# Kernel optimization log

Hardware: AMD Instinct MI355X
Metric: run time of the kernel (lower is better)

Reference implementation:

```python
import jax, jax.numpy as jnp
import numpy as np


def _rconv(x, w, b):
    # reflection-pad 1 then 3x3 valid conv (same spatial size), NCHW/OIHW
    xp = jnp.pad(x, ((0, 0), (0, 0), (1, 1), (1, 1)), mode='reflect')
    y = jax.lax.conv_general_dilated(
        xp, w, window_strides=(1, 1), padding='VALID',
        dimension_numbers=('NCHW', 'OIHW', 'NCHW'))
    return y + b[None, :, None, None]


def setup_inputs() -> dict:
    key = jax.random.key(0)
    ks = jax.random.split(key, 12)
    B, C, H, W = 4, 256, 64, 64
    IC = 128  # inter_channels
    s = lambda fan_in: 1.0 / np.sqrt(fan_in)
    return {
        'query_feat': jax.random.normal(ks[0], (B, C, H, W), jnp.float32),
        'key_feat': jax.random.normal(ks[1], (B, C, H, W), jnp.float32),
        # 1x1 conv projections (stored as [out, in])
        'w_theta': jax.random.normal(ks[2], (IC, C), jnp.float32) * s(C),
        'b_theta': jnp.zeros((IC,), jnp.float32),
        'w_phi': jax.random.normal(ks[3], (IC, C), jnp.float32) * s(C),
        'b_phi': jnp.zeros((IC,), jnp.float32),
        # post-correlation block: conv(1->32), residual(32), conv(32->1)
        'w_in': jax.random.normal(ks[4], (32, 1, 3, 3), jnp.float32) * s(9),
        'b_in': jnp.zeros((32,), jnp.float32),
        'w_r1': jax.random.normal(ks[5], (32, 32, 3, 3), jnp.float32) * s(32 * 9),
        'b_r1': jnp.zeros((32,), jnp.float32),
        'w_r2': jax.random.normal(ks[6], (32, 32, 3, 3), jnp.float32) * s(32 * 9),
        'b_r2': jnp.zeros((32,), jnp.float32),
        'w_out': jax.random.normal(ks[7], (1, 32, 3, 3), jnp.float32) * s(32 * 9),
        'b_out': jnp.zeros((1,), jnp.float32),
    }


def reference(query_feat, key_feat, w_theta, b_theta, w_phi, b_phi,
              w_in, b_in, w_r1, b_r1, w_r2, b_r2, w_out, b_out):
    B, C, H, W = query_feat.shape
    N = H * W
    # 1x1 conv projections, flattened to sequences
    theta = jnp.einsum('oc,bchw->bohw', w_theta, query_feat) + b_theta[None, :, None, None]
    phi = jnp.einsum('oc,bchw->bohw', w_phi, key_feat) + b_phi[None, :, None, None]
    theta = theta.reshape(B, -1, N).transpose(0, 2, 1)  # [B, N, IC]
    phi = phi.reshape(B, -1, N)                          # [B, IC, N]
    # correlation matrix [B, N, N] then max over key positions
    f = jnp.matmul(theta, phi)
    sim = jnp.max(f, axis=-1).reshape(B, 1, H, W)
    # post-correlation conv refinement
    h = _rconv(sim, w_in, b_in)                      # 1 -> 32
    r = jax.nn.relu(_rconv(h, w_r1, b_r1))           # residual block
    r = _rconv(r, w_r2, b_r2)
    h = h + r
    out = _rconv(h, w_out, b_out)                    # 32 -> 1
    return out
```

## Files before the change

### kernel.cpp

```cpp
#include <hip/hip_runtime.h>

#define B_ 4
#define C_ 256
#define HH 64
#define WW 64
#define N_ 4096
#define IC_ 128
#define JC_ 8

typedef __attribute__((ext_vector_type(8))) short bf16x8;
typedef __attribute__((ext_vector_type(4))) float f32x4;

__device__ __forceinline__ short f2bf(float f) {
    unsigned u = __builtin_bit_cast(unsigned, f);
    unsigned r = (u + 0x7FFFu + ((u >> 16) & 1u)) >> 16;
    return (short)r;
}

__device__ __forceinline__ int refl(int v) {
    return v < 0 ? -v : (v > 63 ? 126 - v : v);
}

__global__ __launch_bounds__(256) void k_cvt_w(const float* __restrict__ wt,
                                               const float* __restrict__ wp,
                                               short* __restrict__ wtb,
                                               short* __restrict__ wpb) {
    int i = blockIdx.x * 256 + threadIdx.x;
    wtb[i] = f2bf(wt[i]);
    wpb[i] = f2bf(wp[i]);
}

__global__ __launch_bounds__(256) void k_project(
    const float* __restrict__ qf, const float* __restrict__ kf,
    const short* __restrict__ wq, const short* __restrict__ wk,
    const float* __restrict__ bq, const float* __restrict__ bk,
    short* __restrict__ outq, short* __restrict__ outk) {
    int z = blockIdx.z;
    const float* x = z ? kf : qf;
    const short* wbf = z ? wk : wq;
    const float* bias = z ? bk : bq;
    short* outT = z ? outk : outq;

    int b = blockIdx.y;
    int n0 = blockIdx.x * 64;
    int t = threadIdx.x;
    int lane = t & 63, wv = t >> 6;
    int l15 = lane & 15, q4 = lane >> 4;
    const float* xb = x + (size_t)b * C_ * N_;

    __shared__ float xs[2][32][65];

    f32x4 acc[8];
#pragma unroll
    for (int cf = 0; cf < 8; cf++) acc[cf] = (f32x4){0.f, 0.f, 0.f, 0.f};

    {
        int i0 = t, i1 = t + 256;
        int r0 = i0 >> 4, c0 = i0 & 15;
        int r1 = i1 >> 4, c1 = i1 & 15;
        f32x4 v0 = *(const f32x4*)(xb + (size_t)r0 * N_ + n0 + c0 * 4);
        f32x4 v1 = *(const f32x4*)(xb + (size_t)r1 * N_ + n0 + c1 * 4);
#pragma unroll
        for (int s = 0; s < 4; s++) xs[0][r0][c0 * 4 + s] = v0[s];
#pragma unroll
        for (int s = 0; s < 4; s++) xs[0][r1][c1 * 4 + s] = v1[s];
    }

    for (int ks = 0; ks < 8; ks++) {
        __syncthreads();
        int buf = ks & 1;
        if (ks < 7) {
            int cb = (ks + 1) * 32;
            int i0 = t, i1 = t + 256;
            int r0 = i0 >> 4, c0 = i0 & 15;
            int r1 = i1 >> 4, c1 = i1 & 15;
            f32x4 v0 = *(const f32x4*)(xb + (size_t)(cb + r0) * N_ + n0 + c0 * 4);
            f32x4 v1 = *(const f32x4*)(xb + (size_t)(cb + r1) * N_ + n0 + c1 * 4);
#pragma unroll
            for (int s = 0; s < 4; s++) xs[buf ^ 1][r0][c0 * 4 + s] = v0[s];
#pragma unroll
            for (int s = 0; s < 4; s++) xs[buf ^ 1][r1][c1 * 4 + s] = v1[s];
        }
        int cbase = ks * 32 + q4 * 8;
        bf16x8 a;
#pragma unroll
        for (int j = 0; j < 8; j++) a[j] = f2bf(xs[buf][q4 * 8 + j][wv * 16 + l15]);
#pragma unroll
        for (int cf = 0; cf < 8; cf++) {
            const short* wp = wbf + (cf * 16 + l15) * C_ + cbase;
            bf16x8 bfr = *(const bf16x8*)wp;
            acc[cf] = __builtin_amdgcn_mfma_f32_16x16x32_bf16(a, bfr, acc[cf], 0, 0, 0);
        }
    }
#pragma unroll
    for (int cf = 0; cf < 8; cf++) {
        int ic = cf * 16 + l15;
        float bv = bias[ic];
#pragma unroll
        for (int r = 0; r < 4; r++) {
            int n = n0 + wv * 16 + q4 * 4 + r;
            outT[((size_t)b * N_ + n) * IC_ + ic] = f2bf(acc[cf][r] + bv);
        }
    }
}

__global__ __launch_bounds__(256, 4) void k_corr(const short* __restrict__ thetaT,
                                                 const short* __restrict__ phiT,
                                                 float* __restrict__ simp) {
    __shared__ short ph[2][64][136];

    int b = blockIdx.z, jc = blockIdx.y;
    int i0 = blockIdx.x * 128;
    int t = threadIdx.x;
    int lane = t & 63, w = t >> 6;
    int l15 = lane & 15, q4 = lane >> 4;

    const short* thb = thetaT + ((size_t)b * N_ + i0 + w * 32) * IC_;
    const short* phb = phiT + ((size_t)b * N_ + jc * (N_ / JC_)) * IC_;

    bf16x8 afr[2][4];
#pragma unroll
    for (int rf = 0; rf < 2; rf++)
#pragma unroll
        for (int ks = 0; ks < 4; ks++)
            afr[rf][ks] = *(const bf16x8*)(thb + (size_t)(rf * 16 + l15) * IC_ + ks * 32 + q4 * 8);

    int srow = t >> 4, sc8 = t & 15;
#pragma unroll
    for (int k = 0; k < 4; k++)
        *(bf16x8*)(&ph[0][srow + k * 16][sc8 * 8]) =
            *(const bf16x8*)(phb + (size_t)(srow + k * 16) * IC_ + sc8 * 8);

    f32x4 rmax[2];
#pragma unroll
    for (int rf = 0; rf < 2; rf++) rmax[rf] = (f32x4){-3.0e38f, -3.0e38f, -3.0e38f, -3.0e38f};

    const int NT = (N_ / JC_) / 64;
    for (int it = 0; it < NT; it++) {
        int buf = it & 1;
        __syncthreads();
        if (it < NT - 1) {
            int j0 = (it + 1) * 64;
#pragma unroll
            for (int k = 0; k < 4; k++)
                *(bf16x8*)(&ph[buf ^ 1][srow + k * 16][sc8 * 8]) =
                    *(const bf16x8*)(phb + (size_t)(j0 + srow + k * 16) * IC_ + sc8 * 8);
        }
#pragma unroll
        for (int jf = 0; jf < 4; jf++) {
            bf16x8 bfr[4];
#pragma unroll
            for (int ks = 0; ks < 4; ks++)
                bfr[ks] = *(const bf16x8*)(&ph[buf][jf * 16 + l15][ks * 32 + q4 * 8]);
#pragma unroll
            for (int rf = 0; rf < 2; rf++) {
                f32x4 a2 = (f32x4){0.f, 0.f, 0.f, 0.f};
#pragma unroll
                for (int ks = 0; ks < 4; ks++)
                    a2 = __builtin_amdgcn_mfma_f32_16x16x32_bf16(afr[rf][ks], bfr[ks], a2, 0, 0, 0);
#pragma unroll
                for (int r = 0; r < 4; r++) rmax[rf][r] = fmaxf(rmax[rf][r], a2[r]);
            }
        }
    }

#pragma unroll
    for (int rf = 0; rf < 2; rf++) {
#pragma unroll
        for (int r = 0; r < 4; r++) {
            float v = rmax[rf][r];
            v = fmaxf(v, __shfl_xor(v, 1));
            v = fmaxf(v, __shfl_xor(v, 2));
            v = fmaxf(v, __shfl_xor(v, 4));
            v = fmaxf(v, __shfl_xor(v, 8));
            rmax[rf][r] = v;
        }
    }
    if (l15 == 0) {
        float* sp = simp + ((size_t)(b * JC_ + jc)) * N_ + i0 + w * 32;
#pragma unroll
        for (int rf = 0; rf < 2; rf++)
#pragma unroll
            for (int r = 0; r < 4; r++) sp[rf * 16 + q4 * 4 + r] = rmax[rf][r];
    }
}

__global__ __launch_bounds__(256) void k_conv_in(const float* __restrict__ simp,
                                                 const float* __restrict__ w,
                                                 const float* __restrict__ bias,
                                                 float* __restrict__ h) {
    int y = blockIdx.x, b = blockIdx.y;
    int t = threadIdx.x;
    int oc = t >> 3, x8 = t & 7;
    __shared__ float srow[3][66];
    const float* sb = simp + (size_t)b * JC_ * N_;
    if (t < 192) {
        int r = t >> 6, x = t & 63;
        int idx = refl(y - 1 + r) * 64 + x;
        float v = -3.0e38f;
#pragma unroll
        for (int jc = 0; jc < JC_; jc++) v = fmaxf(v, sb[jc * N_ + idx]);
        srow[r][x + 1] = v;
    }
    if (t < 3) {
        int gy = refl(y - 1 + t);
        float vl = -3.0e38f, vr = -3.0e38f;
#pragma unroll
        for (int jc = 0; jc < JC_; jc++) {
            vl = fmaxf(vl, sb[jc * N_ + gy * 64 + 1]);
            vr = fmaxf(vr, sb[jc * N_ + gy * 64 + 62]);
        }
        srow[t][0] = vl;
        srow[t][65] = vr;
    }
    __syncthreads();

    float wr[9];
#pragma unroll
    for (int k = 0; k < 9; k++) wr[k] = w[oc * 9 + k];
    float bv = bias[oc];
    float acc[8];
#pragma unroll
    for (int xi = 0; xi < 8; xi++) acc[xi] = bv;
#pragma unroll
    for (int ky = 0; ky < 3; ky++)
#pragma unroll
        for (int kx = 0; kx < 3; kx++) {
            float wv2 = wr[ky * 3 + kx];
#pragma unroll
            for (int xi = 0; xi < 8; xi++) acc[xi] += wv2 * srow[ky][x8 * 8 + xi + kx];
        }
    float* op = h + (((size_t)b * 32 + oc) * 64 + y) * 64 + x8 * 8;
#pragma unroll
    for (int xi = 0; xi < 8; xi++) op[xi] = acc[xi];
}

template <bool RELU, bool ADD>
__global__ __launch_bounds__(256) void k_conv_r(const float* __restrict__ in,
                                                const float* __restrict__ w,
                                                const float* __restrict__ bias,
                                                float* __restrict__ out,
                                                const float* __restrict__ add) {
    int y = blockIdx.x, b = blockIdx.z;
    int oc0 = blockIdx.y * 16;
    int t = threadIdx.x;
    __shared__ float tile[32][3][68];

#pragma unroll
    for (int r = 0; r < 3; r++) {
        int gy = refl(y - 1 + r);
#pragma unroll
        for (int i = 0; i < 2; i++) {
            int idx = t + i * 256;
            int ic = idx >> 4, c4 = idx & 15;
            f32x4 v = *(const f32x4*)(in + (((size_t)b * 32 + ic) * 64 + gy) * 64 + c4 * 4);
#pragma unroll
            for (int s = 0; s < 4; s++) tile[ic][r][c4 * 4 + s + 1] = v[s];
        }
    }
    if (t < 96) {
        int ic = t / 3, r = t - ic * 3;
        int gy = refl(y - 1 + r);
        const float* row = in + (((size_t)b * 32 + ic) * 64 + gy) * 64;
        tile[ic][r][0] = row[1];
        tile[ic][r][65] = row[62];
    }
    __syncthreads();

    int oc = oc0 + (t >> 4), x4 = (t & 15) * 4;
    float bv = bias[oc];
    float acc[4];
#pragma unroll
    for (int xi = 0; xi < 4; xi++) acc[xi] = bv;

    for (int ic = 0; ic < 32; ic++) {
        const float* wp = w + ((size_t)oc * 32 + ic) * 9;
        float w0 = wp[0], w1 = wp[1], w2 = wp[2], w3 = wp[3], w4 = wp[4];
        float w5 = wp[5], w6 = wp[6], w7 = wp[7], w8 = wp[8];
        float xr[3][8];
#pragma unroll
        for (int r = 0; r < 3; r++) {
            const float* rowp = &tile[ic][r][x4];
            f32x4 A = *(const f32x4*)(rowp);
            f32x4 Bv = *(const f32x4*)(rowp + 4);
            xr[r][0] = A[0]; xr[r][1] = A[1]; xr[r][2] = A[2]; xr[r][3] = A[3];
            xr[r][4] = Bv[0]; xr[r][5] = Bv[1]; xr[r][6] = Bv[2]; xr[r][7] = Bv[3];
        }
#pragma unroll
        for (int xi = 0; xi < 4; xi++) {
            acc[xi] += w0 * xr[0][xi] + w1 * xr[0][xi + 1] + w2 * xr[0][xi + 2] +
                       w3 * xr[1][xi] + w4 * xr[1][xi + 1] + w5 * xr[1][xi + 2] +
                       w6 * xr[2][xi] + w7 * xr[2][xi + 1] + w8 * xr[2][xi + 2];
        }
    }
    size_t off = (((size_t)b * 32 + oc) * 64 + y) * 64 + x4;
#pragma unroll
    for (int xi = 0; xi < 4; xi++) {
        float v = acc[xi];
        if (RELU) v = fmaxf(v, 0.f);
        if (ADD) v += add[off + xi];
        out[off + xi] = v;
    }
}

__global__ __launch_bounds__(256) void k_conv_out(const float* __restrict__ hb,
                                                  const float* __restrict__ w,
                                                  const float* __restrict__ bias,
                                                  float* __restrict__ outp) {
    int y = blockIdx.x, b = blockIdx.y;
    int t = threadIdx.x;
    int x = t & 63, g = t >> 6;
    __shared__ float red[4][64];
    float acc = 0.f;
#pragma unroll
    for (int i = 0; i < 8; i++) {
        int ic = g * 8 + i;
        const float* wp = w + ic * 9;
#pragma unroll
        for (int ky = 0; ky < 3; ky++) {
            int gy = refl(y + ky - 1);
            const float* row = hb + (((size_t)b * 32 + ic) * 64 + gy) * 64;
#pragma unroll
            for (int kx = 0; kx < 3; kx++) {
                int gx = refl(x + kx - 1);
                acc += wp[ky * 3 + kx] * row[gx];
            }
        }
    }
    red[g][x] = acc;
    __syncthreads();
    if (t < 64) {
        outp[((size_t)b * 64 + y) * 64 + x] =
            bias[0] + red[0][t] + red[1][t] + red[2][t] + red[3][t];
    }
}

extern "C" void kernel_launch(void* const* d_in, const int* in_sizes, int n_in,
                              void* d_out, int out_size, void* d_ws, size_t ws_size,
                              hipStream_t stream) {
    const float* q = (const float*)d_in[0];
    const float* kf = (const float*)d_in[1];
    const float* w_theta = (const float*)d_in[2];
    const float* b_theta = (const float*)d_in[3];
    const float* w_phi = (const float*)d_in[4];
    const float* b_phi = (const float*)d_in[5];
    const float* w_in = (const float*)d_in[6];
    const float* b_in = (const float*)d_in[7];
    const float* w_r1 = (const float*)d_in[8];
    const float* b_r1 = (const float*)d_in[9];
    const float* w_r2 = (const float*)d_in[10];
    const float* b_r2 = (const float*)d_in[11];
    const float* w_out = (const float*)d_in[12];
    const float* b_out = (const float*)d_in[13];
    float* out = (float*)d_out;

    char* ws = (char*)d_ws;
    short* thetaT = (short*)(ws);
    short* phiT = (short*)(ws + 4194304);
    short* wthb = (short*)(ws + 8388608);
    short* wphb = (short*)(ws + 8454144);
    float* simp = (float*)(ws + 8519680);
    float* h = (float*)(ws);
    float* r = (float*)(ws + 2097152);

    k_cvt_w<<<128, 256, 0, stream>>>(w_theta, w_phi, wthb, wphb);
    k_project<<<dim3(64, 4, 2), 256, 0, stream>>>(q, kf, wthb, wphb, b_theta, b_phi,
                                                  thetaT, phiT);
    k_corr<<<dim3(32, JC_, 4), 256, 0, stream>>>(thetaT, phiT, simp);
    k_conv_in<<<dim3(64, 4), 256, 0, stream>>>(simp, w_in, b_in, h);
    k_conv_r<true, false><<<dim3(64, 2, 4), 256, 0, stream>>>(h, w_r1, b_r1, r, nullptr);
    k_conv_r<false, true><<<dim3(64, 2, 4), 256, 0, stream>>>(r, w_r2, b_r2, h, h);
    k_conv_out<<<dim3(64, 4), 256, 0, stream>>>(h, w_out, b_out, out);
}
```

Measured before the change: 167.5 us.

## Fuse weight bf16 conversion into projection and stage conv weights in LDS

```diff
diff --git a/kernel.cpp b/kernel.cpp
--- a/kernel.cpp
+++ b/kernel.cpp
@@ -21,23 +21,14 @@
     return v < 0 ? -v : (v > 63 ? 126 - v : v);
 }
 
-__global__ __launch_bounds__(256) void k_cvt_w(const float* __restrict__ wt,
-                                               const float* __restrict__ wp,
-                                               short* __restrict__ wtb,
-                                               short* __restrict__ wpb) {
-    int i = blockIdx.x * 256 + threadIdx.x;
-    wtb[i] = f2bf(wt[i]);
-    wpb[i] = f2bf(wp[i]);
-}
-
 __global__ __launch_bounds__(256) void k_project(
     const float* __restrict__ qf, const float* __restrict__ kf,
-    const short* __restrict__ wq, const short* __restrict__ wk,
+    const float* __restrict__ wq, const float* __restrict__ wk,
     const float* __restrict__ bq, const float* __restrict__ bk,
     short* __restrict__ outq, short* __restrict__ outk) {
     int z = blockIdx.z;
     const float* x = z ? kf : qf;
-    const short* wbf = z ? wk : wq;
+    const float* wf = z ? wk : wq;
     const float* bias = z ? bk : bq;
     short* outT = z ? outk : outq;
 
@@ -48,7 +39,7 @@
     int l15 = lane & 15, q4 = lane >> 4;
     const float* xb = x + (size_t)b * C_ * N_;
 
-    __shared__ float xs[2][32][65];
+    __shared__ float xs[2][32][68];
 
     f32x4 acc[8];
 #pragma unroll
@@ -58,12 +49,8 @@
         int i0 = t, i1 = t + 256;
         int r0 = i0 >> 4, c0 = i0 & 15;
         int r1 = i1 >> 4, c1 = i1 & 15;
-        f32x4 v0 = *(const f32x4*)(xb + (size_t)r0 * N_ + n0 + c0 * 4);
-        f32x4 v1 = *(const f32x4*)(xb + (size_t)r1 * N_ + n0 + c1 * 4);
-#pragma unroll
-        for (int s = 0; s < 4; s++) xs[0][r0][c0 * 4 + s] = v0[s];
-#pragma unroll
-        for (int s = 0; s < 4; s++) xs[0][r1][c1 * 4 + s] = v1[s];
+        *(f32x4*)(&xs[0][r0][c0 * 4]) = *(const f32x4*)(xb + (size_t)r0 * N_ + n0 + c0 * 4);
+        *(f32x4*)(&xs[0][r1][c1 * 4]) = *(const f32x4*)(xb + (size_t)r1 * N_ + n0 + c1 * 4);
     }
 
     for (int ks = 0; ks < 8; ks++) {
@@ -74,12 +61,10 @@
             int i0 = t, i1 = t + 256;
             int r0 = i0 >> 4, c0 = i0 & 15;
             int r1 = i1 >> 4, c1 = i1 & 15;
-            f32x4 v0 = *(const f32x4*)(xb + (size_t)(cb + r0) * N_ + n0 + c0 * 4);
-            f32x4 v1 = *(const f32x4*)(xb + (size_t)(cb + r1) * N_ + n0 + c1 * 4);
-#pragma unroll
-            for (int s = 0; s < 4; s++) xs[buf ^ 1][r0][c0 * 4 + s] = v0[s];
-#pragma unroll
-            for (int s = 0; s < 4; s++) xs[buf ^ 1][r1][c1 * 4 + s] = v1[s];
+            *(f32x4*)(&xs[buf ^ 1][r0][c0 * 4]) =
+                *(const f32x4*)(xb + (size_t)(cb + r0) * N_ + n0 + c0 * 4);
+            *(f32x4*)(&xs[buf ^ 1][r1][c1 * 4]) =
+                *(const f32x4*)(xb + (size_t)(cb + r1) * N_ + n0 + c1 * 4);
         }
         int cbase = ks * 32 + q4 * 8;
         bf16x8 a;
@@ -87,8 +72,14 @@
         for (int j = 0; j < 8; j++) a[j] = f2bf(xs[buf][q4 * 8 + j][wv * 16 + l15]);
 #pragma unroll
         for (int cf = 0; cf < 8; cf++) {
-            const short* wp = wbf + (cf * 16 + l15) * C_ + cbase;
-            bf16x8 bfr = *(const bf16x8*)wp;
+            const float* wp = wf + (size_t)(cf * 16 + l15) * C_ + cbase;
+            f32x4 wa = *(const f32x4*)wp;
+            f32x4 wb = *(const f32x4*)(wp + 4);
+            bf16x8 bfr;
+            bfr[0] = f2bf(wa[0]); bfr[1] = f2bf(wa[1]);
+            bfr[2] = f2bf(wa[2]); bfr[3] = f2bf(wa[3]);
+            bfr[4] = f2bf(wb[0]); bfr[5] = f2bf(wb[1]);
+            bfr[6] = f2bf(wb[2]); bfr[7] = f2bf(wb[3]);
             acc[cf] = __builtin_amdgcn_mfma_f32_16x16x32_bf16(a, bfr, acc[cf], 0, 0, 0);
         }
     }
@@ -245,6 +236,17 @@
     int oc0 = blockIdx.y * 16;
     int t = threadIdx.x;
     __shared__ float tile[32][3][68];
+    __shared__ float wlds[32 * 16 * 12];
+
+#pragma unroll
+    for (int k = 0; k < 18; k++) {
+        int id = t + k * 256;
+        int ocl = id / 288;
+        int rem = id - ocl * 288;
+        int ic = rem / 9;
+        int tap = rem - ic * 9;
+        wlds[(ic * 16 + ocl) * 12 + tap] = w[(size_t)(oc0 + ocl) * 288 + rem];
+    }
 
 #pragma unroll
     for (int r = 0; r < 3; r++) {
@@ -267,16 +269,21 @@
     }
     __syncthreads();
 
-    int oc = oc0 + (t >> 4), x4 = (t & 15) * 4;
-    float bv = bias[oc];
+    int ocl = t >> 4, x4 = (t & 15) * 4;
+    float bv = bias[oc0 + ocl];
     float acc[4];
 #pragma unroll
     for (int xi = 0; xi < 4; xi++) acc[xi] = bv;
 
+#pragma unroll 2
     for (int ic = 0; ic < 32; ic++) {
-        const float* wp = w + ((size_t)oc * 32 + ic) * 9;
-        float w0 = wp[0], w1 = wp[1], w2 = wp[2], w3 = wp[3], w4 = wp[4];
-        float w5 = wp[5], w6 = wp[6], w7 = wp[7], w8 = wp[8];
+        const float* wr = &wlds[(ic * 16 + ocl) * 12];
+        f32x4 W0 = *(const f32x4*)(wr);
+        f32x4 W1 = *(const f32x4*)(wr + 4);
+        f32x4 W2 = *(const f32x4*)(wr + 8);
+        float w0 = W0[0], w1 = W0[1], w2 = W0[2], w3 = W0[3];
+        float w4 = W1[0], w5 = W1[1], w6 = W1[2], w7 = W1[3];
+        float w8 = W2[0];
         float xr[3][8];
 #pragma unroll
         for (int r = 0; r < 3; r++) {
@@ -293,7 +300,7 @@
                        w6 * xr[2][xi] + w7 * xr[2][xi + 1] + w8 * xr[2][xi + 2];
         }
     }
-    size_t off = (((size_t)b * 32 + oc) * 64 + y) * 64 + x4;
+    size_t off = (((size_t)b * 32 + oc0 + ocl) * 64 + y) * 64 + x4;
 #pragma unroll
     for (int xi = 0; xi < 4; xi++) {
         float v = acc[xi];
@@ -311,11 +318,14 @@
     int t = threadIdx.x;
     int x = t & 63, g = t >> 6;
     __shared__ float red[4][64];
+    __shared__ float wl[288];
+    for (int k = t; k < 288; k += 256) wl[k] = w[k];
+    __syncthreads();
     float acc = 0.f;
 #pragma unroll
     for (int i = 0; i < 8; i++) {
         int ic = g * 8 + i;
-        const float* wp = w + ic * 9;
+        const float* wp = wl + ic * 9;
 #pragma unroll
         for (int ky = 0; ky < 3; ky++) {
             int gy = refl(y + ky - 1);
@@ -357,14 +367,11 @@
     char* ws = (char*)d_ws;
     short* thetaT = (short*)(ws);
     short* phiT = (short*)(ws + 4194304);
-    short* wthb = (short*)(ws + 8388608);
-    short* wphb = (short*)(ws + 8454144);
     float* simp = (float*)(ws + 8519680);
     float* h = (float*)(ws);
     float* r = (float*)(ws + 2097152);
 
-    k_cvt_w<<<128, 256, 0, stream>>>(w_theta, w_phi, wthb, wphb);
-    k_project<<<dim3(64, 4, 2), 256, 0, stream>>>(q, kf, wthb, wphb, b_theta, b_phi,
+    k_project<<<dim3(64, 4, 2), 256, 0, stream>>>(q, kf, w_theta, w_phi, b_theta, b_phi,
                                                   thetaT, phiT);
     k_corr<<<dim3(32, JC_, 4), 256, 0, stream>>>(thetaT, phiT, simp);
     k_conv_in<<<dim3(64, 4), 256, 0, stream>>>(simp, w_in, b_in, h);
```

New measurement: 187.2 us. +11.7%, slower.
